# Kernel optimization log

Hardware: AMD Instinct MI355X
Metric: run time of the kernel (lower is better)

## Reference

```python
import jax, jax.numpy as jnp
import numpy as np

N, E = 100000, 1600000
IN_DIM, OUT_DIM, EDGE_DIM, HEADS = 128, 64, 16, 4
HEAD_DIM = OUT_DIM // HEADS


def setup_inputs() -> dict:
    key = jax.random.key(0)
    ks = jax.random.split(key, 8)
    x = jax.random.normal(ks[0], (N, IN_DIM), dtype=jnp.float32)
    ei = jax.random.randint(ks[1], (2, E), 0, N, dtype=jnp.int32)
    ea = jax.random.normal(ks[2], (E, EDGE_DIM), dtype=jnp.float32)
    # parameters (xavier-ish scaling)
    W_node = jax.random.normal(ks[3], (OUT_DIM, IN_DIM), dtype=jnp.float32) * (1.0 / np.sqrt(IN_DIM))
    W_edge = jax.random.normal(ks[4], (HEADS, EDGE_DIM), dtype=jnp.float32) * (1.0 / np.sqrt(EDGE_DIM))
    att_src = jax.random.normal(ks[5], (1, HEADS, HEAD_DIM), dtype=jnp.float32) * (1.0 / np.sqrt(HEAD_DIM))
    att_dst = jax.random.normal(ks[6], (1, HEADS, HEAD_DIM), dtype=jnp.float32) * (1.0 / np.sqrt(HEAD_DIM))
    bias = jnp.zeros((OUT_DIM,), dtype=jnp.float32)
    return {"x": x, "ei": ei, "ea": ea, "W_node": W_node, "W_edge": W_edge,
            "att_src": att_src, "att_dst": att_dst, "bias": bias}


def reference(x, ei, ea, W_node, W_edge, att_src, att_dst, bias):
    n = x.shape[0]
    Wh = (x @ W_node.T).reshape(n, HEADS, HEAD_DIM)          # [N,H,D]
    s, d = ei[0], ei[1]
    # per-node attention scalars, gathered per edge (avoids gathering Wh[d])
    a_src = jnp.sum(Wh * att_src, axis=-1)                    # [N,H]
    a_dst = jnp.sum(Wh * att_dst, axis=-1)                    # [N,H]
    e = jax.nn.leaky_relu(a_src[s] + a_dst[d] + ea @ W_edge.T, negative_slope=0.2)  # [E,H]
    ex = jnp.exp(e - jnp.max(e))                              # global max, as in torch e.max()
    den = jax.ops.segment_sum(ex, d, num_segments=n)          # [N,H]
    alpha = ex / (den[d] + 1e-9)                              # [E,H]
    msg = Wh[s] * alpha[:, :, None]                           # [E,H,D]
    out = jax.ops.segment_sum(msg, d, num_segments=n)         # [N,H,D]
    return jax.nn.elu(out.reshape(n, OUT_DIM) + bias)
```

## Files before the change

### kernel.cpp

```cpp
#include <hip/hip_runtime.h>
#include <math.h>

#define NN 100000
#define NE 1600000
#define IND 128
#define OUTD 64
#define ED 16
#define NH 4
#define HD 16
#define NB1 98

typedef float f4v __attribute__((ext_vector_type(4)));

__global__ void k_zero(int* __restrict__ deg) {
    int i = blockIdx.x * 256 + threadIdx.x;
    if (i < NN) deg[i] = 0;
}

__global__ __launch_bounds__(512, 6) void k_node(
        const float* __restrict__ x, const float* __restrict__ Wn,
        const float* __restrict__ att_s, const float* __restrict__ att_d,
        float* __restrict__ Wh, float* __restrict__ asrc, float* __restrict__ adst,
        const int* __restrict__ ei, int* __restrict__ deg, int* __restrict__ rnk) {
    __shared__ float4 sWc[64 * 32];
    __shared__ float sx[32][IND];
    int tid = threadIdx.x;
    long long rowBase = (long long)blockIdx.x * 32;

    int e = blockIdx.x * 512 + tid;
    int dd = ei[NE + e];

#pragma unroll
    for (int j = 0; j < 4; j++) {
        int i = tid + j * 512;
        int c = i >> 5, k4 = i & 31;
        sWc[c * 32 + (k4 ^ (c & 7))] = ((const float4*)Wn)[i];
    }
#pragma unroll
    for (int j = 0; j < 2; j++) {
        int i = tid + j * 512;
        int r = i >> 5, k4 = i & 31;
        ((float4*)sx)[r * 32 + k4] = ((const float4*)x)[(rowBase + r) * 32 + k4];
    }
    __syncthreads();

    int wave = tid >> 6, lane = tid & 63;
    float acc0 = 0.f, acc1 = 0.f, acc2 = 0.f, acc3 = 0.f;
    const float4* xr0 = (const float4*)&sx[wave * 4 + 0][0];
    const float4* xr1 = (const float4*)&sx[wave * 4 + 1][0];
    const float4* xr2 = (const float4*)&sx[wave * 4 + 2][0];
    const float4* xr3 = (const float4*)&sx[wave * 4 + 3][0];
    const float4* wrow = &sWc[lane * 32];
    int lx = lane & 7;
#pragma unroll 1
    for (int kk = 0; kk < IND / 16; kk++) {
#pragma unroll
        for (int j = 0; j < 4; j++) {
            int k4 = kk * 4 + j;
            float4 w4 = wrow[k4 ^ lx];
            float4 x0 = xr0[k4], x1 = xr1[k4], x2 = xr2[k4], x3 = xr3[k4];
            acc0 += x0.x * w4.x + x0.y * w4.y + x0.z * w4.z + x0.w * w4.w;
            acc1 += x1.x * w4.x + x1.y * w4.y + x1.z * w4.z + x1.w * w4.w;
            acc2 += x2.x * w4.x + x2.y * w4.y + x2.z * w4.z + x2.w * w4.w;
            acc3 += x3.x * w4.x + x3.y * w4.y + x3.z * w4.z + x3.w * w4.w;
        }
    }
    float as = att_s[lane];
    float ad = att_d[lane];
    float accs[4] = {acc0, acc1, acc2, acc3};
#pragma unroll
    for (int rr = 0; rr < 4; rr++) {
        long long row = rowBase + wave * 4 + rr;
        Wh[row * OUTD + lane] = accs[rr];
        float vs = accs[rr] * as, vd = accs[rr] * ad;
#pragma unroll
        for (int m = 1; m < 16; m <<= 1) {
            vs += __shfl_xor(vs, m);
            vd += __shfl_xor(vd, m);
        }
        if ((lane & 15) == 0) {
            int h = lane >> 4;
            asrc[row * NH + h] = vs;
            adst[row * NH + h] = vd;
        }
    }
    rnk[e] = atomicAdd(&deg[dd], 1);
}

__global__ __launch_bounds__(256) void k_scan1(const int* __restrict__ deg,
                                               int* __restrict__ offA,
                                               int* __restrict__ bsum) {
    __shared__ int sd[256];
    int b = blockIdx.x, t = threadIdx.x;
    int base = b * 1024 + t * 4;
    int v0 = 0, v1 = 0, v2 = 0, v3 = 0;
    if (base + 0 < NN) v0 = deg[base + 0];
    if (base + 1 < NN) v1 = deg[base + 1];
    if (base + 2 < NN) v2 = deg[base + 2];
    if (base + 3 < NN) v3 = deg[base + 3];
    int s = v0 + v1 + v2 + v3;
    sd[t] = s;
    __syncthreads();
    for (int ofs = 1; ofs < 256; ofs <<= 1) {
        int xv = 0;
        if (t >= ofs) xv = sd[t - ofs];
        __syncthreads();
        sd[t] += xv;
        __syncthreads();
    }
    int excl = sd[t] - s;
    if (base + 0 < NN) offA[base + 0] = excl;
    if (base + 1 < NN) offA[base + 1] = excl + v0;
    if (base + 2 < NN) offA[base + 2] = excl + v0 + v1;
    if (base + 3 < NN) offA[base + 3] = excl + v0 + v1 + v2;
    if (t == 255) bsum[b] = sd[255];
}

__global__ __launch_bounds__(128) void k_scan2(int* __restrict__ bsum) {
    __shared__ int sd[128];
    int t = threadIdx.x;
    int v = (t < NB1) ? bsum[t] : 0;
    sd[t] = v;
    __syncthreads();
    for (int ofs = 1; ofs < 128; ofs <<= 1) {
        int xv = 0;
        if (t >= ofs) xv = sd[t - ofs];
        __syncthreads();
        sd[t] += xv;
        __syncthreads();
    }
    if (t < NB1) bsum[t] = sd[t] - v;
}

__global__ void k_scan3(const int* __restrict__ offA, const int* __restrict__ bsum,
                        int* __restrict__ off) {
    int i = blockIdx.x * 256 + threadIdx.x;
    if (i < NN) off[i] = offA[i] + bsum[i >> 10];
    if (i == 0) off[NN] = NE;
}

__global__ __launch_bounds__(256) void k_edge(
        const int* __restrict__ ei, const float* __restrict__ ea,
        const float* __restrict__ We, const float* __restrict__ asrc,
        const float* __restrict__ adst, const int* __restrict__ off,
        const int* __restrict__ rnk, float* __restrict__ rec) {
    __shared__ float sWe[NH * ED];
    if (threadIdx.x < NH * ED) sWe[threadIdx.x] = We[threadIdx.x];
    __syncthreads();
    int e = blockIdx.x * 256 + threadIdx.x;
    int s = ei[e];
    int d = ei[NE + e];
    int r = rnk[e];
    float4 as4 = *(const float4*)(asrc + (long long)s * NH);
    float4 ad4 = *(const float4*)(adst + (long long)d * NH);
    int p = off[d] + r;
    f4v* ea4 = (f4v*)(const_cast<float*>(ea) + (long long)e * ED);
    f4v q0 = __builtin_nontemporal_load(ea4 + 0);
    f4v q1 = __builtin_nontemporal_load(ea4 + 1);
    f4v q2 = __builtin_nontemporal_load(ea4 + 2);
    f4v q3 = __builtin_nontemporal_load(ea4 + 3);
    float asv[4] = {as4.x, as4.y, as4.z, as4.w};
    float adv[4] = {ad4.x, ad4.y, ad4.z, ad4.w};
    unsigned int u[4];
#pragma unroll
    for (int h = 0; h < NH; h++) {
        const float* w = sWe + h * ED;
        float t = asv[h] + adv[h];
        t += q0.x * w[0]  + q0.y * w[1]  + q0.z * w[2]  + q0.w * w[3];
        t += q1.x * w[4]  + q1.y * w[5]  + q1.z * w[6]  + q1.w * w[7];
        t += q2.x * w[8]  + q2.y * w[9]  + q2.z * w[10] + q2.w * w[11];
        t += q3.x * w[12] + q3.y * w[13] + q3.z * w[14] + q3.w * w[15];
        t = (t >= 0.f) ? t : 0.2f * t;
        u[h] = __float_as_uint(expf(t));
    }
    unsigned int ss = (unsigned int)s;
    u[0] = (u[0] & ~31u) | (ss & 31u);
    u[1] = (u[1] & ~15u) | ((ss >> 5) & 15u);
    u[2] = (u[2] & ~15u) | ((ss >> 9) & 15u);
    u[3] = (u[3] & ~15u) | ((ss >> 13) & 15u);
    f4v rv = {__uint_as_float(u[0]), __uint_as_float(u[1]),
              __uint_as_float(u[2]), __uint_as_float(u[3])};
    __builtin_nontemporal_store(rv, (f4v*)rec + p);
}

__global__ __launch_bounds__(256) void k_gather(
        const int* __restrict__ off, float* __restrict__ rec,
        const float* __restrict__ Wh, const float* __restrict__ bias,
        float* __restrict__ out) {
    int node = blockIdx.x * 4 + (threadIdx.x >> 6);
    int lane = threadIdx.x & 63;
    if (node >= NN) return;
    int start = off[node], end = off[node + 1];
    int g = lane >> 4;
    int c16 = lane & 15;
    int h = c16 >> 2;

    float accx = 0.f, accy = 0.f, accz = 0.f, accw = 0.f;
    float dsum = 0.f;
#pragma unroll 2
    for (int j = start + g; j < end; j += 4) {
        f4v r = __builtin_nontemporal_load((f4v*)rec + j);
        unsigned int b0 = __float_as_uint(r.x), b1 = __float_as_uint(r.y);
        unsigned int b2 = __float_as_uint(r.z), b3 = __float_as_uint(r.w);
        int src = (int)((b0 & 31u) | ((b1 & 15u) << 5) | ((b2 & 15u) << 9) | ((b3 & 15u) << 13));
        float ex = (h == 0) ? r.x : (h == 1) ? r.y : (h == 2) ? r.z : r.w;
        float4 w = *(const float4*)(Wh + (long long)src * OUTD + c16 * 4);
        accx += ex * w.x;
        accy += ex * w.y;
        accz += ex * w.z;
        accw += ex * w.w;
        dsum += ex;
    }
#pragma unroll
    for (int m = 16; m < 64; m <<= 1) {
        accx += __shfl_xor(accx, m);
        accy += __shfl_xor(accy, m);
        accz += __shfl_xor(accz, m);
        accw += __shfl_xor(accw, m);
        dsum += __shfl_xor(dsum, m);
    }
    if (g == 0) {
        float rden = 1.0f / (dsum + 1e-9f);
        const float4 b4 = *(const float4*)(bias + c16 * 4);
        float vx = accx * rden + b4.x;
        float vy = accy * rden + b4.y;
        float vz = accz * rden + b4.z;
        float vw = accw * rden + b4.w;
        vx = (vx > 0.f) ? vx : expm1f(vx);
        vy = (vy > 0.f) ? vy : expm1f(vy);
        vz = (vz > 0.f) ? vz : expm1f(vz);
        vw = (vw > 0.f) ? vw : expm1f(vw);
        f4v v = {vx, vy, vz, vw};
        __builtin_nontemporal_store(v, (f4v*)(out + (long long)node * OUTD) + c16);
    }
}

extern "C" void kernel_launch(void* const* d_in, const int* in_sizes, int n_in,
                              void* d_out, int out_size, void* d_ws, size_t ws_size,
                              hipStream_t stream) {
    const float* x     = (const float*)d_in[0];
    const int*   ei    = (const int*)d_in[1];
    const float* ea    = (const float*)d_in[2];
    const float* Wn    = (const float*)d_in[3];
    const float* We    = (const float*)d_in[4];
    const float* att_s = (const float*)d_in[5];
    const float* att_d = (const float*)d_in[6];
    const float* bias  = (const float*)d_in[7];
    float* out = (float*)d_out;

    float* ws   = (float*)d_ws;
    float* Wh   = ws;
    float* asrc = Wh + (size_t)NN * OUTD;
    float* adst = asrc + (size_t)NN * NH;
    float* rec  = adst + (size_t)NN * NH;
    int*   deg  = (int*)(rec + (size_t)NE * 4);
    int*   offA = deg + NN;
    int*   off  = offA + NN;
    int*   bsum = off + NN + 1;
    int*   rnk  = bsum + 128;

    k_zero<<<(NN + 255) / 256, 256, 0, stream>>>(deg);
    k_node<<<NN / 32, 512, 0, stream>>>(x, Wn, att_s, att_d, Wh, asrc, adst,
                                        ei, deg, rnk);
    k_scan1<<<NB1, 256, 0, stream>>>(deg, offA, bsum);
    k_scan2<<<1, 128, 0, stream>>>(bsum);
    k_scan3<<<(NN + 255) / 256, 256, 0, stream>>>(offA, bsum, off);
    k_edge<<<(NE + 255) / 256, 256, 0, stream>>>(ei, ea, We, asrc, adst, off, rnk, rec);
    k_gather<<<(NN + 3) / 4, 256, 0, stream>>>(off, rec, Wh, bias, out);
}
```

Measured before the change: 405.4 us.

## Fuse scan stages via last-block pattern and compute offsets on the fly

Merges the three-kernel exclusive scan into one kernel. Each block writes its partial sum, and the last block to finish, found with an atomic counter and threadfence, scans the block sums. The final offset array is no longer materialised: the edge and gather kernels add the block prefix to the local offset when they use it. This removes two kernel launches and one pass over the node array. In exchange it adds an extra gather load per edge and per node, plus the atomic counter logic.

```diff
diff --git a/kernel.cpp b/kernel.cpp
--- a/kernel.cpp
+++ b/kernel.cpp
@@ -12,9 +12,10 @@
 
 typedef float f4v __attribute__((ext_vector_type(4)));
 
-__global__ void k_zero(int* __restrict__ deg) {
+__global__ void k_zero(int* __restrict__ deg, unsigned int* __restrict__ cnt) {
     int i = blockIdx.x * 256 + threadIdx.x;
     if (i < NN) deg[i] = 0;
+    if (i == 0) *cnt = 0u;
 }
 
 __global__ __launch_bounds__(512, 6) void k_node(
@@ -89,8 +90,10 @@
 
 __global__ __launch_bounds__(256) void k_scan1(const int* __restrict__ deg,
                                                int* __restrict__ offA,
-                                               int* __restrict__ bsum) {
+                                               int* __restrict__ bsum,
+                                               unsigned int* __restrict__ cnt) {
     __shared__ int sd[256];
+    __shared__ unsigned int isLast;
     int b = blockIdx.x, t = threadIdx.x;
     int base = b * 1024 + t * 4;
     int v0 = 0, v1 = 0, v2 = 0, v3 = 0;
@@ -113,37 +116,38 @@
     if (base + 1 < NN) offA[base + 1] = excl + v0;
     if (base + 2 < NN) offA[base + 2] = excl + v0 + v1;
     if (base + 3 < NN) offA[base + 3] = excl + v0 + v1 + v2;
-    if (t == 255) bsum[b] = sd[255];
-}
-
-__global__ __launch_bounds__(128) void k_scan2(int* __restrict__ bsum) {
-    __shared__ int sd[128];
-    int t = threadIdx.x;
-    int v = (t < NB1) ? bsum[t] : 0;
-    sd[t] = v;
-    __syncthreads();
-    for (int ofs = 1; ofs < 128; ofs <<= 1) {
-        int xv = 0;
-        if (t >= ofs) xv = sd[t - ofs];
+    if (t == 255) {
+        bsum[b] = sd[255];
+        __threadfence();
+        isLast = (atomicAdd(cnt, 1u) == NB1 - 1) ? 1u : 0u;
+    }
+    __syncthreads();
+    if (isLast) {
+        __shared__ int sb[128];
+        int v = 0;
+        if (t < 128) {
+            v = (t < NB1) ? atomicAdd(&bsum[t], 0) : 0;
+            sb[t] = v;
+        }
         __syncthreads();
-        sd[t] += xv;
-        __syncthreads();
-    }
-    if (t < NB1) bsum[t] = sd[t] - v;
-}
-
-__global__ void k_scan3(const int* __restrict__ offA, const int* __restrict__ bsum,
-                        int* __restrict__ off) {
-    int i = blockIdx.x * 256 + threadIdx.x;
-    if (i < NN) off[i] = offA[i] + bsum[i >> 10];
-    if (i == 0) off[NN] = NE;
+        for (int ofs = 1; ofs < 128; ofs <<= 1) {
+            int xv = 0;
+            if (t >= ofs && t < 128) xv = sb[t - ofs];
+            __syncthreads();
+            if (t < 128) sb[t] += xv;
+            __syncthreads();
+        }
+        if (t < NB1) bsum[t] = sb[t] - v;
+        if (t == 0) *cnt = 0u;
+    }
 }
 
 __global__ __launch_bounds__(256) void k_edge(
         const int* __restrict__ ei, const float* __restrict__ ea,
         const float* __restrict__ We, const float* __restrict__ asrc,
-        const float* __restrict__ adst, const int* __restrict__ off,
-        const int* __restrict__ rnk, float* __restrict__ rec) {
+        const float* __restrict__ adst, const int* __restrict__ offA,
+        const int* __restrict__ bsum, const int* __restrict__ rnk,
+        float* __restrict__ rec) {
     __shared__ float sWe[NH * ED];
     if (threadIdx.x < NH * ED) sWe[threadIdx.x] = We[threadIdx.x];
     __syncthreads();
@@ -153,7 +157,7 @@
     int r = rnk[e];
     float4 as4 = *(const float4*)(asrc + (long long)s * NH);
     float4 ad4 = *(const float4*)(adst + (long long)d * NH);
-    int p = off[d] + r;
+    int p = offA[d] + bsum[d >> 10] + r;
     f4v* ea4 = (f4v*)(const_cast<float*>(ea) + (long long)e * ED);
     f4v q0 = __builtin_nontemporal_load(ea4 + 0);
     f4v q1 = __builtin_nontemporal_load(ea4 + 1);
@@ -184,13 +188,14 @@
 }
 
 __global__ __launch_bounds__(256) void k_gather(
-        const int* __restrict__ off, float* __restrict__ rec,
-        const float* __restrict__ Wh, const float* __restrict__ bias,
-        float* __restrict__ out) {
+        const int* __restrict__ offA, const int* __restrict__ bsum,
+        float* __restrict__ rec, const float* __restrict__ Wh,
+        const float* __restrict__ bias, float* __restrict__ out) {
     int node = blockIdx.x * 4 + (threadIdx.x >> 6);
     int lane = threadIdx.x & 63;
     if (node >= NN) return;
-    int start = off[node], end = off[node + 1];
+    int start = offA[node] + bsum[node >> 10];
+    int end = (node + 1 < NN) ? offA[node + 1] + bsum[(node + 1) >> 10] : NE;
     int g = lane >> 4;
     int c16 = lane & 15;
     int h = c16 >> 2;
@@ -255,16 +260,15 @@
     float* rec  = adst + (size_t)NN * NH;
     int*   deg  = (int*)(rec + (size_t)NE * 4);
     int*   offA = deg + NN;
-    int*   off  = offA + NN;
-    int*   bsum = off + NN + 1;
+    int*   bsum = offA + NN;
     int*   rnk  = bsum + 128;
-
-    k_zero<<<(NN + 255) / 256, 256, 0, stream>>>(deg);
+    unsigned int* cnt = (unsigned int*)(rnk + NE);
+
+    k_zero<<<(NN + 255) / 256, 256, 0, stream>>>(deg, cnt);
     k_node<<<NN / 32, 512, 0, stream>>>(x, Wn, att_s, att_d, Wh, asrc, adst,
                                         ei, deg, rnk);
-    k_scan1<<<NB1, 256, 0, stream>>>(deg, offA, bsum);
-    k_scan2<<<1, 128, 0, stream>>>(bsum);
-    k_scan3<<<(NN + 255) / 256, 256, 0, stream>>>(offA, bsum, off);
-    k_edge<<<(NE + 255) / 256, 256, 0, stream>>>(ei, ea, We, asrc, adst, off, rnk, rec);
-    k_gather<<<(NN + 3) / 4, 256, 0, stream>>>(off, rec, Wh, bias, out);
-}
+    k_scan1<<<NB1, 256, 0, stream>>>(deg, offA, bsum, cnt);
+    k_edge<<<(NE + 255) / 256, 256, 0, stream>>>(ei, ea, We, asrc, adst,
+                                                 offA, bsum, rnk, rec);
+    k_gather<<<(NN + 3) / 4, 256, 0, stream>>>(offA, bsum, rec, Wh, bias, out);
+}
```

Result: no change. 406.9 us (+0.4%).
